# Kernel optimization log

Measured on AMD Instinct MI355X. Metric: run time of the kernel, lower is better.

## Reference

```python
import jax, jax.numpy as jnp
import numpy as np

L, Q = 200, 21          # alignment length, number of Potts states (20 AAs + gap)
REG_H, REG_J = 0.01, 0.01  # L2 regularization strengths (reg_h, reg_J)
M = 1024                # number of sequences in the MSA


def setup_inputs() -> dict:
    key = jax.random.key(0)
    ks = jax.random.split(key, 6)
    X_tokens = jax.random.randint(ks[0], (M, L), 0, Q)
    weights = jax.random.uniform(ks[1], (M,), dtype=jnp.float32)
    fi = jax.random.uniform(ks[2], (L, Q), dtype=jnp.float32)
    fi_target = fi / fi.sum(axis=1, keepdims=True)  # single-site frequencies
    fij = jax.random.uniform(ks[3], (L, Q, L, Q), dtype=jnp.float32)
    fij_target = fij / fij.sum(axis=(1, 3), keepdims=True)  # pairwise frequencies
    h = jax.random.normal(ks[4], (L, Q), dtype=jnp.float32) * 1e-4
    J = jax.random.normal(ks[5], (L, Q, L, Q), dtype=jnp.float32) * 1e-4
    # remove_autocorr: zero self-couplings J[i,:,i,:]
    eye = jnp.eye(L, dtype=jnp.float32)[:, None, :, None]
    J = J * (1.0 - eye)
    return {"X_tokens": X_tokens, "weights": weights, "fi_target": fi_target,
            "fij_target": fij_target, "h": h, "J": J}


def _loss_third(X, weights, fi_target, fij_target, h, J):
    # loss_third_fn: sites i in [2L//3, L)
    start = 2 * L // 3
    w = weights / weights.sum()
    sites = jnp.arange(start, L)                         # (S,)
    causal = (jnp.arange(L)[None, :] < sites[:, None])   # (S, L), j < i mask
    Jm = J[start:] * causal[:, None, :, None].astype(J.dtype)  # (S, q, L, q)
    # energy_i = fi[i] @ h[i] + sum_{j<i} J[i,:,j,:] * fij[i,:,j,:], summed over i
    energy = (jnp.einsum('ia,ia->', fi_target[start:], h[start:])
              + jnp.einsum('iajb,iajb->', Jm, fij_target[start:]))
    # logits[n,i,a] = h[i,a] + sum_{j<i,b} J[i,a,j,b] * X[n,j,b]
    logits = jnp.einsum('njb,iajb->nia', X, Jm) + h[start:][None]  # (M, S, q)
    logZ = jax.scipy.special.logsumexp(logits, axis=-1)            # (M, S)
    nll = -(energy - jnp.einsum('ni,n->', logZ, w))
    loss = nll + REG_H * jnp.sum(h * h) + REG_J * jnp.sum(J * J)
    return loss, nll


def reference(X_tokens, weights, fi_target, fij_target, h, J):
    X = jax.nn.one_hot(X_tokens, Q, dtype=jnp.float32)  # (M, L, q)
    return _loss_third(X, weights, fi_target, fij_target, h, J)
```

## Files before the change

kernel.cpp:

```cpp
#include <hip/hip_runtime.h>
#include <cstdint>

#define LL    200
#define QQ    21
#define MM    1024
#define START 133
#define NS    67
#define RGH   0.01f
#define RGJ   0.01f


#define LOGITS_OFF 256
#define LOGITS_BYTES ((size_t)NS * QQ * MM * 4)
#define TOKT_OFF (LOGITS_OFF + LOGITS_BYTES)
#define WS_NEED (TOKT_OFF + (size_t)LL * MM * 4)

__device__ __forceinline__ int row_off(int r) { return r * 24 + ((r & 7) << 2); }
#define LDSJ_FLOATS 16160

__device__ __forceinline__ float block_reduce_sum(float v) {
  __shared__ float sm[4];
  #pragma unroll
  for (int off = 32; off > 0; off >>= 1) v += __shfl_down(v, off, 64);
  const int lane = threadIdx.x & 63;
  const int wv   = threadIdx.x >> 6;
  __syncthreads();
  if (lane == 0) sm[wv] = v;
  __syncthreads();
  float r = 0.0f;
  if (threadIdx.x == 0) r = sm[0] + sm[1] + sm[2] + sm[3];
  return r;
}

__global__ __launch_bounds__(256) void kern_jsum(
    const float* __restrict__ J, const float* __restrict__ fij,
    float* __restrict__ acc) {
  const int i = blockIdx.x;
  const size_t base4 = (size_t)i * (QQ * LL * QQ / 4);
  const float4* __restrict__ J4 = (const float4*)J + base4;
  const float4* __restrict__ F4 = (const float4*)fij + base4;
  const int total4 = QQ * LL * QQ / 4;
  const int lim = i * QQ;
  const bool act = (i >= START);
  float j2 = 0.0f, e = 0.0f;
  for (int f = blockIdx.y * 256 + threadIdx.x; f < total4;
       f += 256 * gridDim.y) {
    const float4 v = J4[f];
    j2 += v.x * v.x + v.y * v.y + v.z * v.z + v.w * v.w;
    if (act) {
      const int a   = f / 1050;
      const int pos = (f - a * 1050) * 4;
      if (pos + 3 < lim) {
        const float4 u = F4[f];
        e += v.x * u.x + v.y * u.y + v.z * u.z + v.w * u.w;
      } else if (pos < lim) {
        const float* vf = (const float*)&v;
        const float* uf = (const float*)(F4 + f);
        for (int k = 0; k < 4 && pos + k < lim; ++k) e += vf[k] * uf[k];
      }
    }
  }
  const float tj2 = block_reduce_sum(j2);
  const float te  = block_reduce_sum(e);
  if (threadIdx.x == 0) {
    atomicAdd(acc + 0, tj2);
    if (act) atomicAdd(acc + 1, te);
  }
}

__global__ __launch_bounds__(256) void kern_tokT(
    const int* __restrict__ X, int* __restrict__ tokT) {
  const int idx = blockIdx.x * 256 + threadIdx.x;
  if (idx < LL * MM) {
    const int j = idx / MM;
    const int n = idx - j * MM;
    tokT[idx] = X[n * LL + j];
  }
}

__global__ __launch_bounds__(512) void kern_logz_p1(
    const float* __restrict__ J, const int* __restrict__ tokT,
    float* __restrict__ logits) {
  __shared__ __align__(16) float ldsJ[LDSJ_FLOATS];
  const int i  = START + blockIdx.x;
  const int j0 = blockIdx.z * 64;
  if (j0 >= i) return;
  const int t = threadIdx.x;
  const int n = blockIdx.y * 512 + t;

  float lg[QQ];
  #pragma unroll
  for (int a = 0; a < QQ; ++a) lg[a] = 0.0f;

  const float* Ji = J + (size_t)i * (QQ * LL * QQ);

  #pragma unroll
  for (int s = 0; s < 2; ++s) {
    const int jb = j0 + 32 * s;
    if (jb >= i) break;
    const int tj  = min(32, i - jb);
    const int cnt = tj * QQ;
    __syncthreads();
    for (int a = 0; a < QQ; ++a) {
      const float* src = Ji + a * (LL * QQ) + jb * QQ;
      for (int idx = t; idx < cnt; idx += 512) {
        const int jl = idx / QQ;
        const int b  = idx - jl * QQ;
        ldsJ[row_off(jl * QQ + b) + a] = src[idx];
      }
    }
    __syncthreads();
    for (int jl = 0; jl < tj; ++jl) {
      const int b = tokT[(jb + jl) * MM + n];
      const float* row = &ldsJ[row_off(jl * QQ + b)];
      const float4* r4 = (const float4*)row;
      const float4 q0 = r4[0], q1 = r4[1], q2 = r4[2], q3 = r4[3], q4 = r4[4];
      const float q5 = row[20];
      lg[0]  += q0.x; lg[1]  += q0.y; lg[2]  += q0.z; lg[3]  += q0.w;
      lg[4]  += q1.x; lg[5]  += q1.y; lg[6]  += q1.z; lg[7]  += q1.w;
      lg[8]  += q2.x; lg[9]  += q2.y; lg[10] += q2.z; lg[11] += q2.w;
      lg[12] += q3.x; lg[13] += q3.y; lg[14] += q3.z; lg[15] += q3.w;
      lg[16] += q4.x; lg[17] += q4.y; lg[18] += q4.z; lg[19] += q4.w;
      lg[20] += q5;
    }
  }

  float* dst = logits + (size_t)blockIdx.x * QQ * MM + n;
  #pragma unroll
  for (int a = 0; a < QQ; ++a) atomicAdd(dst + a * MM, lg[a]);
}

__global__ __launch_bounds__(256) void kern_logz_p2(
    const float* __restrict__ logits, const float* __restrict__ h,
    const float* __restrict__ w, float* __restrict__ acc) {
  const int iI = blockIdx.x;
  const int i  = START + iI;
  const int t  = threadIdx.x;
  const int n  = blockIdx.y * 256 + t;
  const float* hi = h + i * QQ;
  const float* src = logits + (size_t)iI * QQ * MM + n;
  float lg[QQ];
  float mx = -3.0e38f;
  #pragma unroll
  for (int a = 0; a < QQ; ++a) {
    lg[a] = src[a * MM] + hi[a];
    mx = fmaxf(mx, lg[a]);
  }
  float s = 0.0f;
  #pragma unroll
  for (int a = 0; a < QQ; ++a) s += expf(lg[a] - mx);
  const float contrib = w[n] * (mx + logf(s));
  const float tot = block_reduce_sum(contrib);
  if (t == 0) atomicAdd(acc + 2, tot);
}

__global__ __launch_bounds__(256) void kern_logz_mono(
    const float* __restrict__ J, const int* __restrict__ Xtok,
    const float* __restrict__ h, const float* __restrict__ w,
    float* __restrict__ acc) {
  __shared__ __align__(16) float ldsJ[LDSJ_FLOATS];
  const int i = START + blockIdx.x;
  const int t = threadIdx.x;
  const int n = blockIdx.y * 256 + t;
  float lg[QQ];
  #pragma unroll
  for (int a = 0; a < QQ; ++a) lg[a] = 0.0f;
  const float* Ji = J + (size_t)i * (QQ * LL * QQ);
  for (int j0 = 0; j0 < i; j0 += 32) {
    const int tj  = min(32, i - j0);
    const int cnt = tj * QQ;
    __syncthreads();
    for (int a = 0; a < QQ; ++a) {
      const float* src = Ji + a * (LL * QQ) + j0 * QQ;
      for (int idx = t; idx < cnt; idx += 256) {
        const int jl = idx / QQ;
        const int b  = idx - jl * QQ;
        ldsJ[row_off(jl * QQ + b) + a] = src[idx];
      }
    }
    __syncthreads();
    for (int jl = 0; jl < tj; ++jl) {
      const int b = Xtok[n * LL + (j0 + jl)];
      const float* row = &ldsJ[row_off(jl * QQ + b)];
      #pragma unroll
      for (int a = 0; a < QQ; ++a) lg[a] += row[a];
    }
  }
  const float* hi = h + i * QQ;
  float mx = -3.0e38f;
  #pragma unroll
  for (int a = 0; a < QQ; ++a) { lg[a] += hi[a]; mx = fmaxf(mx, lg[a]); }
  float s = 0.0f;
  #pragma unroll
  for (int a = 0; a < QQ; ++a) s += expf(lg[a] - mx);
  const float contrib = w[n] * (mx + logf(s));
  const float tot = block_reduce_sum(contrib);
  if (t == 0) atomicAdd(acc + 2, tot);
}

__global__ __launch_bounds__(256) void kern_final(
    const float* __restrict__ h, const float* __restrict__ fi,
    const float* __restrict__ w, const float* __restrict__ acc,
    float* __restrict__ out) {
  const int t = threadIdx.x;
  float hs = 0.0f, eh = 0.0f, ws = 0.0f;
  for (int idx = t; idx < LL * QQ; idx += 256) {
    const float hv = h[idx];
    hs += hv * hv;
    if (idx >= START * QQ) eh += fi[idx] * hv;
  }
  for (int idx = t; idx < MM; idx += 256) ws += w[idx];
  const float ths = block_reduce_sum(hs);
  const float teh = block_reduce_sum(eh);
  const float tws = block_reduce_sum(ws);
  if (t == 0) {
    const float energy = teh + acc[1];
    const float nll = acc[2] / tws - energy;
    out[0] = nll + RGH * ths + RGJ * acc[0];
    out[1] = nll;
  }
}

extern "C" void kernel_launch(void* const* d_in, const int* in_sizes, int n_in,
                              void* d_out, int out_size, void* d_ws, size_t ws_size,
                              hipStream_t stream) {
  const int*   Xtok = (const int*)  d_in[0];
  const float* wts  = (const float*)d_in[1];
  const float* fi   = (const float*)d_in[2];
  const float* fij  = (const float*)d_in[3];
  const float* h    = (const float*)d_in[4];
  const float* J    = (const float*)d_in[5];
  float* out    = (float*)d_out;
  float* acc    = (float*)d_ws;
  float* logits = (float*)((char*)d_ws + LOGITS_OFF);
  int*   tokT   = (int*)  ((char*)d_ws + TOKT_OFF);

  if (ws_size >= WS_NEED) {
    hipMemsetAsync(d_ws, 0, TOKT_OFF, stream);
    kern_tokT<<<(LL * MM + 255) / 256, 256, 0, stream>>>(Xtok, tokT);
    kern_jsum<<<dim3(LL, 4), 256, 0, stream>>>(J, fij, acc);
    kern_logz_p1<<<dim3(NS, 2, 4), 512, 0, stream>>>(J, tokT, logits);
    kern_logz_p2<<<dim3(NS, 4), 256, 0, stream>>>(logits, h, wts, acc);
    kern_final<<<1, 256, 0, stream>>>(h, fi, wts, acc, out);
  } else {
    hipMemsetAsync(d_ws, 0, 256, stream);
    kern_jsum<<<dim3(LL, 4), 256, 0, stream>>>(J, fij, acc);
    kern_logz_mono<<<dim3(NS, 4), 256, 0, stream>>>(J, Xtok, h, wts, acc);
    kern_final<<<1, 256, 0, stream>>>(h, fi, wts, acc, out);
  }
}
```

Before: 253.8 us.

## Re-split jsum and logZ kernels across more blocks with smaller J tiles

kern_jsum now launches one block per (i,a) row instead of four strided blocks per site. That removes per-element division and spreads the 34 MB J/fij stream over many more blocks. kern_logz_p1 uses 16-wide j tiles over 13 z-slices with a single LDS fill, a padded stride-22 row layout, and float2 accumulators. kern_logz_p2 uses 64-thread blocks with a wave-only reduction. The cost is more blocks and more atomics to the logits buffer and accumulators.

```diff
diff --git a/kernel.cpp b/kernel.cpp
--- a/kernel.cpp
+++ b/kernel.cpp
@@ -9,14 +9,14 @@
 #define RGH   0.01f
 #define RGJ   0.01f
 
-
 #define LOGITS_OFF 256
 #define LOGITS_BYTES ((size_t)NS * QQ * MM * 4)
 #define TOKT_OFF (LOGITS_OFF + LOGITS_BYTES)
 #define WS_NEED (TOKT_OFF + (size_t)LL * MM * 4)
 
-__device__ __forceinline__ int row_off(int r) { return r * 24 + ((r & 7) << 2); }
-#define LDSJ_FLOATS 16160
+#define RSTRIDE 22
+#define TJ 16
+#define LDSJ_FLOATS (TJ * QQ * RSTRIDE)
 
 __device__ __forceinline__ float block_reduce_sum(float v) {
   __shared__ float sm[4];
@@ -36,28 +36,25 @@
     const float* __restrict__ J, const float* __restrict__ fij,
     float* __restrict__ acc) {
   const int i = blockIdx.x;
-  const size_t base4 = (size_t)i * (QQ * LL * QQ / 4);
-  const float4* __restrict__ J4 = (const float4*)J + base4;
-  const float4* __restrict__ F4 = (const float4*)fij + base4;
-  const int total4 = QQ * LL * QQ / 4;
-  const int lim = i * QQ;
+  const int a = blockIdx.y;
+  const size_t rb = (size_t)i * (QQ * LL * QQ) + (size_t)a * (LL * QQ);
+  const float4* __restrict__ J4 = (const float4*)(J + rb);
+  const float4* __restrict__ F4 = (const float4*)(fij + rb);
   const bool act = (i >= START);
+  const int lim  = act ? i * QQ : 0;
+  const int lim4 = lim >> 2;
+  const int rem  = lim & 3;
   float j2 = 0.0f, e = 0.0f;
-  for (int f = blockIdx.y * 256 + threadIdx.x; f < total4;
-       f += 256 * gridDim.y) {
+  for (int f = threadIdx.x; f < (LL * QQ / 4); f += 256) {
     const float4 v = J4[f];
     j2 += v.x * v.x + v.y * v.y + v.z * v.z + v.w * v.w;
-    if (act) {
-      const int a   = f / 1050;
-      const int pos = (f - a * 1050) * 4;
-      if (pos + 3 < lim) {
-        const float4 u = F4[f];
-        e += v.x * u.x + v.y * u.y + v.z * u.z + v.w * u.w;
-      } else if (pos < lim) {
-        const float* vf = (const float*)&v;
-        const float* uf = (const float*)(F4 + f);
-        for (int k = 0; k < 4 && pos + k < lim; ++k) e += vf[k] * uf[k];
-      }
+    if (f < lim4) {
+      const float4 u = F4[f];
+      e += v.x * u.x + v.y * u.y + v.z * u.z + v.w * u.w;
+    } else if (f == lim4 && rem) {
+      const float* vf = (const float*)&v;
+      const float* uf = (const float*)(F4 + f);
+      for (int k = 0; k < rem; ++k) e += vf[k] * uf[k];
     }
   }
   const float tj2 = block_reduce_sum(j2);
@@ -78,66 +75,60 @@
   }
 }
 
-__global__ __launch_bounds__(512) void kern_logz_p1(
+__global__ __launch_bounds__(512, 8) void kern_logz_p1(
     const float* __restrict__ J, const int* __restrict__ tokT,
     float* __restrict__ logits) {
-  __shared__ __align__(16) float ldsJ[LDSJ_FLOATS];
+  __shared__ float ldsJ[LDSJ_FLOATS];
   const int i  = START + blockIdx.x;
-  const int j0 = blockIdx.z * 64;
+  const int j0 = blockIdx.z * TJ;
   if (j0 >= i) return;
-  const int t = threadIdx.x;
-  const int n = blockIdx.y * 512 + t;
-
-  float lg[QQ];
-  #pragma unroll
-  for (int a = 0; a < QQ; ++a) lg[a] = 0.0f;
-
-  const float* Ji = J + (size_t)i * (QQ * LL * QQ);
-
-  #pragma unroll
-  for (int s = 0; s < 2; ++s) {
-    const int jb = j0 + 32 * s;
-    if (jb >= i) break;
-    const int tj  = min(32, i - jb);
-    const int cnt = tj * QQ;
-    __syncthreads();
-    for (int a = 0; a < QQ; ++a) {
-      const float* src = Ji + a * (LL * QQ) + jb * QQ;
-      for (int idx = t; idx < cnt; idx += 512) {
-        const int jl = idx / QQ;
-        const int b  = idx - jl * QQ;
-        ldsJ[row_off(jl * QQ + b) + a] = src[idx];
-      }
-    }
-    __syncthreads();
-    for (int jl = 0; jl < tj; ++jl) {
-      const int b = tokT[(jb + jl) * MM + n];
-      const float* row = &ldsJ[row_off(jl * QQ + b)];
-      const float4* r4 = (const float4*)row;
-      const float4 q0 = r4[0], q1 = r4[1], q2 = r4[2], q3 = r4[3], q4 = r4[4];
-      const float q5 = row[20];
-      lg[0]  += q0.x; lg[1]  += q0.y; lg[2]  += q0.z; lg[3]  += q0.w;
-      lg[4]  += q1.x; lg[5]  += q1.y; lg[6]  += q1.z; lg[7]  += q1.w;
-      lg[8]  += q2.x; lg[9]  += q2.y; lg[10] += q2.z; lg[11] += q2.w;
-      lg[12] += q3.x; lg[13] += q3.y; lg[14] += q3.z; lg[15] += q3.w;
-      lg[16] += q4.x; lg[17] += q4.y; lg[18] += q4.z; lg[19] += q4.w;
-      lg[20] += q5;
-    }
+  const int t    = threadIdx.x;
+  const int n    = blockIdx.y * 512 + t;
+  const int tj   = min(TJ, i - j0);
+  const int tj21 = tj * QQ;
+
+  const float* Ji = J + (size_t)i * (QQ * LL * QQ) + j0 * QQ;
+  for (int idx = t; idx < TJ * QQ * QQ; idx += 512) {
+    const int a   = idx / (TJ * QQ);
+    const int rem = idx - a * (TJ * QQ);
+    if (rem < tj21) ldsJ[rem * RSTRIDE + a] = Ji[a * (LL * QQ) + rem];
+  }
+  __syncthreads();
+
+  float2 lg2[10];
+  #pragma unroll
+  for (int k = 0; k < 10; ++k) lg2[k] = make_float2(0.0f, 0.0f);
+  float lg20 = 0.0f;
+
+  for (int jl = 0; jl < tj; ++jl) {
+    const int b = tokT[(j0 + jl) * MM + n];
+    const int r = (jl * QQ + b) * RSTRIDE;
+    const float2* row2 = (const float2*)&ldsJ[r];
+    #pragma unroll
+    for (int k = 0; k < 10; ++k) {
+      const float2 v = row2[k];
+      lg2[k].x += v.x;
+      lg2[k].y += v.y;
+    }
+    lg20 += ldsJ[r + 20];
   }
 
   float* dst = logits + (size_t)blockIdx.x * QQ * MM + n;
   #pragma unroll
-  for (int a = 0; a < QQ; ++a) atomicAdd(dst + a * MM, lg[a]);
-}
-
-__global__ __launch_bounds__(256) void kern_logz_p2(
+  for (int k = 0; k < 10; ++k) {
+    atomicAdd(dst + (2 * k) * MM, lg2[k].x);
+    atomicAdd(dst + (2 * k + 1) * MM, lg2[k].y);
+  }
+  atomicAdd(dst + 20 * MM, lg20);
+}
+
+__global__ __launch_bounds__(64) void kern_logz_p2(
     const float* __restrict__ logits, const float* __restrict__ h,
     const float* __restrict__ w, float* __restrict__ acc) {
   const int iI = blockIdx.x;
   const int i  = START + iI;
-  const int t  = threadIdx.x;
-  const int n  = blockIdx.y * 256 + t;
-  const float* hi = h + i * QQ;
+  const int n  = blockIdx.y * 64 + threadIdx.x;
+  const float* hi  = h + i * QQ;
   const float* src = logits + (size_t)iI * QQ * MM + n;
   float lg[QQ];
   float mx = -3.0e38f;
@@ -149,16 +140,18 @@
   float s = 0.0f;
   #pragma unroll
   for (int a = 0; a < QQ; ++a) s += expf(lg[a] - mx);
-  const float contrib = w[n] * (mx + logf(s));
-  const float tot = block_reduce_sum(contrib);
-  if (t == 0) atomicAdd(acc + 2, tot);
-}
-
+  float v = w[n] * (mx + logf(s));
+  #pragma unroll
+  for (int off = 32; off > 0; off >>= 1) v += __shfl_down(v, off, 64);
+  if (threadIdx.x == 0) atomicAdd(acc + 2, v);
+}
+
+#define LDSJ_MONO (32 * QQ * RSTRIDE)
 __global__ __launch_bounds__(256) void kern_logz_mono(
     const float* __restrict__ J, const int* __restrict__ Xtok,
     const float* __restrict__ h, const float* __restrict__ w,
     float* __restrict__ acc) {
-  __shared__ __align__(16) float ldsJ[LDSJ_FLOATS];
+  __shared__ float ldsJ[LDSJ_MONO];
   const int i = START + blockIdx.x;
   const int t = threadIdx.x;
   const int n = blockIdx.y * 256 + t;
@@ -173,15 +166,13 @@
     for (int a = 0; a < QQ; ++a) {
       const float* src = Ji + a * (LL * QQ) + j0 * QQ;
       for (int idx = t; idx < cnt; idx += 256) {
-        const int jl = idx / QQ;
-        const int b  = idx - jl * QQ;
-        ldsJ[row_off(jl * QQ + b) + a] = src[idx];
+        ldsJ[idx * RSTRIDE + a] = src[idx];
       }
     }
     __syncthreads();
     for (int jl = 0; jl < tj; ++jl) {
       const int b = Xtok[n * LL + (j0 + jl)];
-      const float* row = &ldsJ[row_off(jl * QQ + b)];
+      const float* row = &ldsJ[(jl * QQ + b) * RSTRIDE];
       #pragma unroll
       for (int a = 0; a < QQ; ++a) lg[a] += row[a];
     }
@@ -238,13 +229,13 @@
   if (ws_size >= WS_NEED) {
     hipMemsetAsync(d_ws, 0, TOKT_OFF, stream);
     kern_tokT<<<(LL * MM + 255) / 256, 256, 0, stream>>>(Xtok, tokT);
-    kern_jsum<<<dim3(LL, 4), 256, 0, stream>>>(J, fij, acc);
-    kern_logz_p1<<<dim3(NS, 2, 4), 512, 0, stream>>>(J, tokT, logits);
-    kern_logz_p2<<<dim3(NS, 4), 256, 0, stream>>>(logits, h, wts, acc);
+    kern_jsum<<<dim3(LL, QQ), 256, 0, stream>>>(J, fij, acc);
+    kern_logz_p1<<<dim3(NS, 2, 13), 512, 0, stream>>>(J, tokT, logits);
+    kern_logz_p2<<<dim3(NS, 16), 64, 0, stream>>>(logits, h, wts, acc);
     kern_final<<<1, 256, 0, stream>>>(h, fi, wts, acc, out);
   } else {
     hipMemsetAsync(d_ws, 0, 256, stream);
-    kern_jsum<<<dim3(LL, 4), 256, 0, stream>>>(J, fij, acc);
+    kern_jsum<<<dim3(LL, QQ), 256, 0, stream>>>(J, fij, acc);
     kern_logz_mono<<<dim3(NS, 4), 256, 0, stream>>>(J, Xtok, h, wts, acc);
     kern_final<<<1, 256, 0, stream>>>(h, fi, wts, acc, out);
   }
```

Result: slower. 297.8 us (+17.3%).
